# Performance work log

Hardware: AMD Instinct MI355X
Metric: run time of the kernel (lower is better)

The kernel has to match this reference:

```python
import jax, jax.numpy as jnp
import numpy as np

B, C, H, W = 256, 2048, 16, 8
NUM_CLASSES = 10000
SCALE = 1.0  # cls_layer.s for cls_type='Linear', scale=1
N_ITERS = 20


def setup_inputs() -> dict:
    key = jax.random.key(0)
    k1, k2, k3 = jax.random.split(key, 3)
    features = jax.random.normal(k1, (B, C, H, W), dtype=jnp.float32)
    targets = jax.random.randint(k2, (B,), 0, NUM_CLASSES)
    # nn.init.normal_(self.weight, std=0.01)
    weight = jax.random.normal(k3, (NUM_CLASSES, C), dtype=jnp.float32) * 0.01
    return {"features": features, "targets": targets, "weight": weight}


def reference(features, targets, weight):
    # 1) GlobalAvgPool over H,W then squeeze -> [B, C]; bottleneck is identity
    #    (embedding_dim=0, with_bnneck=False).
    neck_feat = features.mean(axis=(2, 3))
    t = neck_feat.shape[0]

    # cls_type == 'Linear': logits = F.linear(neck_feat, weight); cls_layer is
    # a pass-through, so every loop iteration computes identical quantities
    # (the random 'maskarea' in the original is overwritten before use).
    logits = jnp.einsum('bc,nc->bn', neck_feat, weight)  # [B, num_classes]
    soft = jax.nn.softmax(logits, axis=1)

    # right_prob = softmax probability at the target class (scatter+mul+sum)
    right_prob = jnp.take_along_axis(soft, targets[:, None], axis=1)[:, 0]  # [t]

    # All N_ITERS iterations append the same right_prob, so at the final
    # iteration: mean == right_prob, variance over iterations == 0.
    mean_sl = right_prob                      # [t]
    var_sl = jnp.zeros_like(right_prob)       # [t]
    con = mean_sl / (var_sl * 1e4)            # -> +inf (matches torch div-by-0)
    ri = jnp.tanh(1.2 * con)                  # tanh(inf) = 1.0
    # new_weight[i] = t * ri[i] / ri.sum()
    new_weight = (t * ri / ri.sum())[None, :]  # [1, t]

    cls_outputs = logits                       # Linear cls layer is identity
    pred_class_logits = logits * SCALE
    feat = neck_feat                           # neck_feat == 'before', bottleneck identity
    return cls_outputs, pred_class_logits, feat, new_weight
```

## Files before the change

kernel.cpp:

```cpp
#include <hip/hip_runtime.h>


#define OUT1_OFF (256 * 10000)
#define FEAT_OFF (2 * 256 * 10000)
#define NW_OFF   (2 * 256 * 10000 + 256 * 2048)

typedef __attribute__((ext_vector_type(4))) float f32x4;
typedef __attribute__((ext_vector_type(8))) short bf16x8;
typedef __attribute__((ext_vector_type(4))) unsigned int u32x4;

__device__ inline unsigned pk2bf(float lo, float hi) {
    unsigned a = __float_as_uint(lo), b = __float_as_uint(hi);
    unsigned ra = (a + 0x7FFFu + ((a >> 16) & 1u)) >> 16;
    unsigned rb = (b + 0x7FFFu + ((b >> 16) & 1u)) & 0xFFFF0000u;
    return ra | rb;
}

__device__ inline void gload_lds16(const void* g, void* l) {
    __builtin_amdgcn_global_load_lds(
        (const __attribute__((address_space(1))) void*)g,
        (__attribute__((address_space(3))) void*)l, 16, 0, 0);
}

__global__ __launch_bounds__(256) void prep_kernel(
    const float* __restrict__ f, const float* __restrict__ W,
    float* __restrict__ out, unsigned int* __restrict__ wsA32,
    u32x4* __restrict__ wsB) {
    int bid = blockIdx.x;
    int tid = threadIdx.x;
    if (bid < 32768) {
        int g = tid >> 5;
        int l = tid & 31;
        int r0 = bid * 16 + g * 2;
        const f32x4* s0 = (const f32x4*)(f + (size_t)r0 * 128);
        f32x4 v0 = s0[l];
        f32x4 v1 = s0[l + 32];
        float a = v0[0] + v0[1] + v0[2] + v0[3];
        float b = v1[0] + v1[1] + v1[2] + v1[3];
#pragma unroll
        for (int off = 16; off >= 1; off >>= 1) {
            a += __shfl_xor(a, off);
            b += __shfl_xor(b, off);
        }
        if (l == 0) {
            float m0 = a * (1.0f / 128.0f), m1 = b * (1.0f / 128.0f);
            float2 fv; fv.x = m0; fv.y = m1;
            *(float2*)&out[FEAT_OFF + r0] = fv;
            int bb = r0 >> 11, c = r0 & 2047;
            int chunk = ((bb >> 4) * 256 + (c >> 3)) * 16 + (bb & 15);
            wsA32[chunk * 4 + ((c & 7) >> 1)] = pk2bf(m0, m1);
        }
        if (bid == 0) out[NW_OFF + tid] = 1.0f;
    } else {
        int nb = bid - 32768;
        int n0 = nb * 16;
        int r = tid & 15, kq = tid >> 4;
        const f32x4* src = (const f32x4*)(W + (size_t)(n0 + r) * 2048) + kq * 2;
        u32x4* dst = wsB + ((size_t)(n0 >> 4) * 256 + kq) * 16 + r;
#pragma unroll
        for (int kc = 0; kc < 16; ++kc) {
            f32x4 a = src[kc * 32], b = src[kc * 32 + 1];
            u32x4 p;
            p.x = pk2bf(a[0], a[1]);
            p.y = pk2bf(a[2], a[3]);
            p.z = pk2bf(b[0], b[1]);
            p.w = pk2bf(b[2], b[3]);
            dst[kc * 256] = p;
        }
    }
}

__global__ __launch_bounds__(512) void gemm_kernel(
    const u32x4* __restrict__ A16, const u32x4* __restrict__ B16,
    float* __restrict__ out) {
    __shared__ u32x4 As[3][1024];
    __shared__ u32x4 Bs[3][512];

    int tid = threadIdx.x;
    int mh = blockIdx.x;
    int n0 = blockIdx.y * 64;
    int wid = tid >> 6, lane = tid & 63;
    int wm = wid >> 1, wn = wid & 1;
    int r = lane & 15, kqu = lane >> 4;

    const u32x4* ga[2];
#pragma unroll
    for (int i = 0; i < 2; ++i) {
        int ci = tid + i * 512;
        ga[i] = A16 + (((mh * 8 + (ci >> 7)) * 256 + ((ci >> 4) & 7)) * 16 + (ci & 15));
    }
    const u32x4* gb = B16 + ((size_t)(n0 >> 4) * 4096 + (tid >> 7) * 4096 + (tid & 127));

    f32x4 acc[2][2];
#pragma unroll
    for (int i = 0; i < 2; ++i)
#pragma unroll
        for (int j = 0; j < 2; ++j) acc[i][j] = (f32x4){0.f, 0.f, 0.f, 0.f};

#define STAGE(kt, buf)                                                \
    {                                                                 \
        _Pragma("unroll") for (int i = 0; i < 2; ++i)                 \
            gload_lds16(ga[i] + (kt) * 128, &As[buf][tid + i * 512]); \
        gload_lds16(gb + (kt) * 128, &Bs[buf][tid]);                  \
    }

    STAGE(0, 0);
    STAGE(1, 1);
    asm volatile("s_waitcnt vmcnt(3)" ::: "memory");
    __builtin_amdgcn_sched_barrier(0);
    __builtin_amdgcn_s_barrier();
    __builtin_amdgcn_sched_barrier(0);

    for (int kt = 0; kt < 32; ++kt) {
        int cur = kt % 3;
        if (kt <= 29) {
            int nx2 = (kt + 2) % 3;
            STAGE(kt + 2, nx2);
        }
#pragma unroll
        for (int ks = 0; ks < 2; ++ks) {
            int kcl = ks * 4 + kqu;
            bf16x8 av[2], bv[2];
#pragma unroll
            for (int i = 0; i < 2; ++i)
                av[i] = *(const bf16x8*)&As[cur][(wm * 2 + i) * 128 + kcl * 16 + r];
#pragma unroll
            for (int j = 0; j < 2; ++j)
                bv[j] = *(const bf16x8*)&Bs[cur][(wn * 2 + j) * 128 + kcl * 16 + r];
#pragma unroll
            for (int i = 0; i < 2; ++i)
#pragma unroll
                for (int j = 0; j < 2; ++j)
                    acc[i][j] = __builtin_amdgcn_mfma_f32_16x16x32_bf16(
                        av[i], bv[j], acc[i][j], 0, 0, 0);
        }
        if (kt <= 29) { asm volatile("s_waitcnt vmcnt(3)" ::: "memory"); }
        else          { asm volatile("s_waitcnt vmcnt(0)" ::: "memory"); }
        __builtin_amdgcn_sched_barrier(0);
        if (kt < 31) {
            __builtin_amdgcn_s_barrier();
        }
        __builtin_amdgcn_sched_barrier(0);
    }

#pragma unroll
    for (int i = 0; i < 2; ++i)
#pragma unroll
        for (int j = 0; j < 2; ++j) {
            int n = n0 + (wn * 2 + j) * 16 + r;
            if (n < 10000) {
                int mbase = mh * 128 + (wm * 2 + i) * 16 + kqu * 4;
#pragma unroll
                for (int q = 0; q < 4; ++q) {
                    float v = acc[i][j][q];
                    size_t off = (size_t)(mbase + q) * 10000 + n;
                    out[off] = v;
                    out[OUT1_OFF + off] = v;
                }
            }
        }
#undef STAGE
}

extern "C" void kernel_launch(void* const* d_in, const int* in_sizes, int n_in,
                              void* d_out, int out_size, void* d_ws, size_t ws_size,
                              hipStream_t stream) {
    const float* feats = (const float*)d_in[0];
    const float* weight = (const float*)d_in[2];
    float* out = (float*)d_out;
    unsigned int* wsA = (unsigned int*)d_ws;
    u32x4* wsB = (u32x4*)((char*)d_ws + (2u << 20));

    prep_kernel<<<33393, 256, 0, stream>>>(feats, weight, out, wsA, wsB);
    gemm_kernel<<<dim3(2, 157), 512, 0, stream>>>((const u32x4*)wsA, wsB, out);
}
```

Baseline: 113.0 us.

## Stage A tiles through registers and swap grid axis order in GEMM

The A operand is no longer copied into shared memory by direct global-to-LDS DMA. It is loaded into registers two stages ahead and written to LDS just before each barrier; B keeps using the direct DMA path. The grid is also transposed so that blockIdx.x walks the N tiles and blockIdx.y selects the M half, which changes the order blocks are dispatched in and how cache is shared. This adds register pressure and explicit LDS writes plus lgkmcnt waits on the critical path, in exchange for possibly cheaper A staging.

Measured after the change: 123.2 us. +9.0%, slower.

```diff
diff --git a/kernel.cpp b/kernel.cpp
--- a/kernel.cpp
+++ b/kernel.cpp
@@ -77,8 +77,8 @@
     __shared__ u32x4 Bs[3][512];
 
     int tid = threadIdx.x;
-    int mh = blockIdx.x;
-    int n0 = blockIdx.y * 64;
+    int n0 = blockIdx.x * 64;
+    int mh = blockIdx.y;
     int wid = tid >> 6, lane = tid & 63;
     int wm = wid >> 1, wn = wid & 1;
     int r = lane & 15, kqu = lane >> 4;
@@ -97,16 +97,28 @@
 #pragma unroll
         for (int j = 0; j < 2; ++j) acc[i][j] = (f32x4){0.f, 0.f, 0.f, 0.f};
 
-#define STAGE(kt, buf)                                                \
-    {                                                                 \
-        _Pragma("unroll") for (int i = 0; i < 2; ++i)                 \
-            gload_lds16(ga[i] + (kt) * 128, &As[buf][tid + i * 512]); \
-        gload_lds16(gb + (kt) * 128, &Bs[buf][tid]);                  \
+    u32x4 RX0, RX1, RY0, RY1;
+
+#define ALOAD(kt, R0_, R1_)      \
+    {                            \
+        R0_ = ga[0][(kt) * 128]; \
+        R1_ = ga[1][(kt) * 128]; \
     }
+#define AWRITE(buf, R0_, R1_)    \
+    {                            \
+        As[buf][tid] = R0_;      \
+        As[buf][tid + 512] = R1_;\
+    }
+#define BDMA(kt, buf) gload_lds16(gb + (kt) * 128, &Bs[buf][tid]);
 
-    STAGE(0, 0);
-    STAGE(1, 1);
-    asm volatile("s_waitcnt vmcnt(3)" ::: "memory");
+    ALOAD(0, RX0, RX1);
+    BDMA(0, 0);
+    ALOAD(1, RY0, RY1);
+    BDMA(1, 1);
+    asm volatile("s_waitcnt vmcnt(1)" ::: "memory");
+    __builtin_amdgcn_sched_barrier(0);
+    AWRITE(0, RX0, RX1);
+    asm volatile("s_waitcnt lgkmcnt(0)" ::: "memory");
     __builtin_amdgcn_sched_barrier(0);
     __builtin_amdgcn_s_barrier();
     __builtin_amdgcn_sched_barrier(0);
@@ -115,7 +127,9 @@
         int cur = kt % 3;
         if (kt <= 29) {
             int nx2 = (kt + 2) % 3;
-            STAGE(kt + 2, nx2);
+            if (kt & 1) { ALOAD(kt + 2, RY0, RY1); }
+            else        { ALOAD(kt + 2, RX0, RX1); }
+            BDMA(kt + 2, nx2);
         }
 #pragma unroll
         for (int ks = 0; ks < 2; ++ks) {
@@ -134,10 +148,15 @@
                     acc[i][j] = __builtin_amdgcn_mfma_f32_16x16x32_bf16(
                         av[i], bv[j], acc[i][j], 0, 0, 0);
         }
-        if (kt <= 29) { asm volatile("s_waitcnt vmcnt(3)" ::: "memory"); }
-        else          { asm volatile("s_waitcnt vmcnt(0)" ::: "memory"); }
+        if (kt <= 29)      { asm volatile("s_waitcnt vmcnt(3)" ::: "memory"); }
+        else if (kt == 30) { asm volatile("s_waitcnt vmcnt(0)" ::: "memory"); }
         __builtin_amdgcn_sched_barrier(0);
-        if (kt < 31) {
+        if (kt <= 30) {
+            int nx1 = (kt + 1) % 3;
+            if (kt & 1) { AWRITE(nx1, RX0, RX1); }
+            else        { AWRITE(nx1, RY0, RY1); }
+            asm volatile("s_waitcnt lgkmcnt(0)" ::: "memory");
+            __builtin_amdgcn_sched_barrier(0);
             __builtin_amdgcn_s_barrier();
         }
         __builtin_amdgcn_sched_barrier(0);
@@ -159,7 +178,9 @@
                 }
             }
         }
-#undef STAGE
+#undef ALOAD
+#undef AWRITE
+#undef BDMA
 }
 
 extern "C" void kernel_launch(void* const* d_in, const int* in_sizes, int n_in,
@@ -172,5 +193,5 @@
     u32x4* wsB = (u32x4*)((char*)d_ws + (2u << 20));
 
     prep_kernel<<<33393, 256, 0, stream>>>(feats, weight, out, wsA, wsB);
-    gemm_kernel<<<dim3(2, 157), 512, 0, stream>>>((const u32x4*)wsA, wsB, out);
+    gemm_kernel<<<dim3(157, 2), 512, 0, stream>>>((const u32x4*)wsA, wsB, out);
 }
```
